# Kernel tuning notes

Hardware: AMD Instinct MI355X
Metric: run time of the kernel (lower is better)

The kernel has to match this reference:

```python
import jax, jax.numpy as jnp
import numpy as np

EMBED_DIM = 1024
NUM_HEADS = 16
HEAD_DIM = EMBED_DIM // NUM_HEADS
LAMBDA_ENTANGLE = 0.35


def setup_inputs() -> dict:
    key = jax.random.key(0)
    ks = jax.random.split(key, 10)
    B, S, D = 2, 2048, EMBED_DIM
    init = 1.0 / np.sqrt(D)  # mimic nn.Linear uniform init scale
    x = jax.random.normal(ks[0], (B, S, D), dtype=jnp.float32)
    Wq = jax.random.uniform(ks[1], (D, D), jnp.float32, -init, init)
    bq = jax.random.uniform(ks[2], (D,), jnp.float32, -init, init)
    Wk = jax.random.uniform(ks[3], (D, D), jnp.float32, -init, init)
    bk = jax.random.uniform(ks[4], (D,), jnp.float32, -init, init)
    Wv = jax.random.uniform(ks[5], (D, D), jnp.float32, -init, init)
    bv = jax.random.uniform(ks[6], (D,), jnp.float32, -init, init)
    Wo = jax.random.uniform(ks[7], (D, D), jnp.float32, -init, init)
    bo = jax.random.uniform(ks[8], (D,), jnp.float32, -init, init)
    J_attn = jax.random.normal(ks[9], (NUM_HEADS, HEAD_DIM, HEAD_DIM), dtype=jnp.float32) * 0.02
    lambda_attn = jnp.asarray(LAMBDA_ENTANGLE, dtype=jnp.float32)
    return {"x": x, "Wq": Wq, "bq": bq, "Wk": Wk, "bk": bk, "Wv": Wv, "bv": bv,
            "Wo": Wo, "bo": bo, "J_attn": J_attn, "lambda_attn": lambda_attn}


def reference(x, Wq, bq, Wk, bk, Wv, bv, Wo, bo, J_attn, lambda_attn):
    B, S, D = x.shape
    H, Hd = NUM_HEADS, HEAD_DIM
    scale = jnp.sqrt(jnp.asarray(Hd, dtype=x.dtype))

    def heads(W, b):
        # (B,S,D) @ (D,D) + b -> (B,H,S,Hd)
        y = jnp.einsum('bsd,ed->bse', x, W) + b
        return y.reshape(B, S, H, Hd).transpose(0, 2, 1, 3)

    Q = heads(Wq, bq)
    K = heads(Wk, bk)
    V = heads(Wv, bv)

    scores = jnp.einsum('bhid,bhjd->bhij', Q, K) / scale
    # bilinear entanglement correction: tanh(Q) J tanh(K)^T
    QJ = jnp.einsum('bhid,hde->bhie', jnp.tanh(Q), J_attn)  # (B,H,S,Hd)
    delta = jnp.einsum('bhie,bhje->bhij', QJ, jnp.tanh(K))
    scores = scores + lambda_attn * delta

    causal = jnp.triu(jnp.ones((S, S), dtype=bool), k=1)
    scores = jnp.where(causal, -jnp.inf, scores)

    probs = jax.nn.softmax(scores, axis=-1)
    out = jnp.einsum('bhij,bhjd->bhid', probs, V)  # (B,H,S,Hd)
    out = out.transpose(0, 2, 1, 3).reshape(B, S, D)
    return jnp.einsum('bsd,ed->bse', out, Wo) + bo
```

## Files before the change

### kernel.cpp

```cpp
#include <hip/hip_runtime.h>
#include <hip/hip_bf16.h>

typedef unsigned short u16;
typedef __bf16 bf16x8 __attribute__((ext_vector_type(8)));
typedef float f32x4 __attribute__((ext_vector_type(4)));
typedef unsigned short u16x4 __attribute__((ext_vector_type(4)));

#define MFMA16(a, b, c) __builtin_amdgcn_mfma_f32_16x16x32_bf16(a, b, c, 0, 0, 0)

#define EMB 1024
#define SEQ 2048
#define NH 16
#define HD 64
#define LOG2E 1.4426950408889634f

#define GLOAD_LDS16(g, l) __builtin_amdgcn_global_load_lds( \
    (const __attribute__((address_space(1))) unsigned int*)(g), \
    (__attribute__((address_space(3))) unsigned int*)(l), 16, 0, 0)

__device__ __forceinline__ float b2f(u16 u) {
    union { unsigned int i; float f; } v; v.i = ((unsigned int)u) << 16; return v.f;
}
__device__ __forceinline__ u16 f2b(float f) {
    __hip_bfloat16 h = __float2bfloat16(f);
    return *reinterpret_cast<u16*>(&h);
}
__device__ __forceinline__ u16x4 pack4(float a, float b, float c, float d) {
    union { __hip_bfloat162 h2[2]; u16x4 u; } r;
    r.h2[0] = __float22bfloat162_rn(float2{a, b});
    r.h2[1] = __float22bfloat162_rn(float2{c, d});
    return r.u;
}
__device__ __forceinline__ bf16x8 ldfrag(const u16* p) {
    return *reinterpret_cast<const bf16x8*>(p);
}
__device__ __forceinline__ bf16x8 cvt8(const float* p) {
    const float4 a = *reinterpret_cast<const float4*>(p);
    const float4 b = *reinterpret_cast<const float4*>(p + 4);
    union { u16x4 q[2]; bf16x8 v; } r;
    r.q[0] = pack4(a.x, a.y, a.z, a.w);
    r.q[1] = pack4(b.x, b.y, b.z, b.w);
    return r.v;
}
__device__ __forceinline__ float fast_tanh(float x) {
    float t = __builtin_amdgcn_exp2f(x * (2.0f * LOG2E));
    return 1.0f - 2.0f * __builtin_amdgcn_rcpf(t + 1.0f);
}

__global__ __launch_bounds__(256) void cvt_all(
        const float* __restrict__ x,  const float* __restrict__ Wq,
        const float* __restrict__ Wk, const float* __restrict__ Wv,
        const float* __restrict__ Wo, const float* __restrict__ J,
        u16* __restrict__ dst)
{
    size_t i = ((size_t)blockIdx.x * 256 + threadIdx.x) * 8;
    const float* src; size_t off; u16* d;
    if (i < 4194304) { src = x; off = i; d = dst + i; }
    else if (i < 8388608) {
        size_t j = i - 4194304; int w = (int)(j >> 20); off = j & 1048575;
        src = (w == 0) ? Wq : (w == 1) ? Wk : (w == 2) ? Wv : Wo;
        d = dst + i;
    } else {
        off = i - 8388608; src = J; d = dst + 29360128 + off;
    }
    *(bf16x8*)d = cvt8(src + off);
}

template<int MI>
__global__ __launch_bounds__(256, 4) void gemm_epi(
        const u16* __restrict__ A,
        const u16* __restrict__ W0, const float* __restrict__ B0,
        const u16* __restrict__ W1, const float* __restrict__ B1,
        const u16* __restrict__ W2, const float* __restrict__ B2,
        const float* __restrict__ lam, const u16* __restrict__ Jb,
        u16* __restrict__ Qa, u16* __restrict__ Ka, u16* __restrict__ Vt,
        float* __restrict__ out, int modeBase)
{
    const int mode = modeBase + blockIdx.z;
    const u16* W; const float* bias;
    if (blockIdx.z == 0)      { W = W0; bias = B0; }
    else if (blockIdx.z == 1) { W = W1; bias = B1; }
    else                      { W = W2; bias = B2; }

    __shared__ __attribute__((aligned(16))) u16 sA[MI * 32 * 64];
    __shared__ __attribute__((aligned(16))) u16 sB[128 * 64];

    const int t = threadIdx.x;
    const int w = t >> 6, L = t & 63;
    const int wm = w >> 1, wn = w & 1;
    const int lr = L & 15, lq = L >> 4;
    const int wbase = t & 192;
    const int m0 = blockIdx.y * (MI * 32), n0 = blockIdx.x * 128;

    f32x4 acc[MI][4];
#pragma unroll
    for (int i = 0; i < MI; i++)
#pragma unroll
        for (int j = 0; j < 4; j++) { f32x4 z = {0.f, 0.f, 0.f, 0.f}; acc[i][j] = z; }

    for (int k0 = 0; k0 < EMB; k0 += 64) {
        __syncthreads();
#pragma unroll
        for (int q = 0; q < MI; q++) {
            int c = q * 256 + t;
            int row = c >> 3, cc = c & 7;
            int col8 = cc ^ (row & 7);
            GLOAD_LDS16(&A[(size_t)(m0 + row) * EMB + k0 + col8 * 8],
                        &sA[(q * 256 + wbase) * 8]);
        }
#pragma unroll
        for (int q = 0; q < 4; q++) {
            int c = q * 256 + t;
            int row = c >> 3, cc = c & 7;
            int col8 = cc ^ (row & 7);
            GLOAD_LDS16(&W[(size_t)(n0 + row) * EMB + k0 + col8 * 8],
                        &sB[(q * 256 + wbase) * 8]);
        }
        __syncthreads();
#pragma unroll
        for (int s = 0; s < 2; s++) {
            bf16x8 af[MI], bfr[4];
#pragma unroll
            for (int mi = 0; mi < MI; mi++) {
                int row = wm * (MI * 16) + mi * 16 + lr;
                af[mi] = ldfrag(&sA[(row * 8 + ((s * 4 + lq) ^ (row & 7))) * 8]);
            }
#pragma unroll
            for (int ni = 0; ni < 4; ni++) {
                int row = wn * 64 + ni * 16 + lr;
                bfr[ni] = ldfrag(&sB[(row * 8 + ((s * 4 + lq) ^ (row & 7))) * 8]);
            }
#pragma unroll
            for (int mi = 0; mi < MI; mi++)
#pragma unroll
                for (int ni = 0; ni < 4; ni++)
                    acc[mi][ni] = MFMA16(bfr[ni], af[mi], acc[mi][ni]);
        }
    }

    if (mode == 1) __syncthreads();
    u16* sU = (w < 2) ? &sA[(size_t)w * 4096] : &sB[(size_t)(w - 2) * 4096];

    const float lamf = lam[0];
    const float qsc = 0.125f * LOG2E, lsc = lamf * LOG2E;
#pragma unroll
    for (int mi = 0; mi < MI; mi++)
#pragma unroll
        for (int ni = 0; ni < 4; ni++) {
            const int sg = m0 + wm * (MI * 16) + mi * 16 + lr;
            const int ng = n0 + wn * 64 + ni * 16 + lq * 4;
            const float4 bv4 = *(const float4*)&bias[ng];
            const float v0 = acc[mi][ni][0] + bv4.x;
            const float v1 = acc[mi][ni][1] + bv4.y;
            const float v2 = acc[mi][ni][2] + bv4.z;
            const float v3 = acc[mi][ni][3] + bv4.w;
            if (mode == 3) {
                float4 o = {v0, v1, v2, v3};
                *(float4*)&out[(size_t)sg * EMB + ng] = o;
            } else {
                const int b = sg >> 11, s0 = sg & 2047;
                const int h = ng >> 6, d0 = ng & 63;
                if (mode == 0) {
                    size_t i128 = ((size_t)(b * NH + h) * SEQ + s0) * 128 + d0;
                    *(u16x4*)&Qa[i128] = pack4(v0 * qsc, v1 * qsc, v2 * qsc, v3 * qsc);
                    *(u16x4*)&Qa[i128 + 64] =
                        pack4(lsc * fast_tanh(v0), lsc * fast_tanh(v1),
                              lsc * fast_tanh(v2), lsc * fast_tanh(v3));
                } else if (mode == 1) {
                    *(u16x4*)&Ka[((size_t)(b * NH + h) * SEQ + s0) * 128 + d0] =
                        pack4(v0, v1, v2, v3);
                    const int sl = mi * 16 + lr;
                    const int chunk = (d0 >> 3) ^ (sl & 7);
                    *(u16x4*)&sU[sl * 64 + chunk * 8 + (d0 & 7)] =
                        pack4(fast_tanh(v0), fast_tanh(v1),
                              fast_tanh(v2), fast_tanh(v3));
                } else {
#pragma unroll
                    for (int r = 0; r < 4; r++) {
                        float vr = (r == 0) ? v0 : (r == 1) ? v1 : (r == 2) ? v2 : v3;
                        Vt[((size_t)(b * NH + h) * HD + d0 + r) * SEQ + s0] = f2b(vr);
                    }
                }
            }
        }

    if (mode == 1) {
        const int hn = (n0 >> 6) + wn;
        const u16* Jh = Jb + (size_t)hn * 4096;
        bf16x8 jf[4][2];
#pragma unroll
        for (int nt = 0; nt < 4; nt++)
#pragma unroll
            for (int s2 = 0; s2 < 2; s2++)
                jf[nt][s2] = ldfrag(&Jh[(nt * 16 + lr) * 64 + s2 * 32 + lq * 8]);
#pragma unroll
        for (int rt2 = 0; rt2 < 4; rt2++) {
            int r64 = rt2 * 16 + lr;
            bf16x8 a0 = ldfrag(&sU[r64 * 64 + ((0 + lq) ^ (r64 & 7)) * 8]);
            bf16x8 a1 = ldfrag(&sU[r64 * 64 + ((4 + lq) ^ (r64 & 7)) * 8]);
            const int grow = m0 + wm * 64 + rt2 * 16 + lr;
            const int bb = grow >> 11, ss = grow & 2047;
            const size_t kbase = ((size_t)(bb * NH + hn) * SEQ + ss) * 128 + 64;
#pragma unroll
            for (int nt = 0; nt < 4; nt++) {
                f32x4 acc2 = {0.f, 0.f, 0.f, 0.f};
                acc2 = MFMA16(jf[nt][0], a0, acc2);
                acc2 = MFMA16(jf[nt][1], a1, acc2);
                *(u16x4*)&Ka[kbase + nt * 16 + lq * 4] =
                    pack4(acc2[0], acc2[1], acc2[2], acc2[3]);
            }
        }
    }
}

__global__ __launch_bounds__(512) void flash(
        const u16* __restrict__ Qa, const u16* __restrict__ Ka,
        const u16* __restrict__ Vt, u16* __restrict__ attn)
{
    __shared__ __attribute__((aligned(16))) u16 sK[2][128 * 128];
    __shared__ __attribute__((aligned(16))) u16 sVt[2][64 * 128];
    __shared__ __attribute__((aligned(16))) u16 sP[128 * 136];
    __shared__ float sLs[2][4][64][2];

    const int t = threadIdx.x, w = t >> 6, L = t & 63, lr = L & 15, lq = L >> 4;
    const int wq = w & 3, wk = w >> 2;
    const int bh = blockIdx.x & 31, p = blockIdx.x >> 5;
    const int i_l = wq * 16 + lr;
    const u16* Kbase = Ka + (size_t)bh * SEQ * 128;
    const u16* Vbase = Vt + (size_t)bh * HD * SEQ;
    const int b = bh >> 4, h = bh & 15;
    float* sOt = reinterpret_cast<float*>(sK);

    const u16* kq[4];
#pragma unroll
    for (int q = 0; q < 4; q++) {
        int c = q * 512 + t;
        int row = c >> 4, cc = c & 15;
        kq[q] = Kbase + (size_t)row * 128 + (cc ^ (row & 15)) * 8;
    }
    const u16* vq[2];
#pragma unroll
    for (int q = 0; q < 2; q++) {
        int c = q * 512 + t;
        int d = c >> 4, cc = c & 15;
        vq[q] = Vbase + (size_t)d * SEQ + (cc ^ (d & 7)) * 8;
    }

#pragma unroll 1
    for (int seg = 0; seg < 2; seg++) {
        const int qt = seg ? 15 - p : p;
        const int qm = qt * 128;

        bf16x8 qf[2][4];
#pragma unroll
        for (int g = 0; g < 2; g++) {
            const u16* qrow = Qa + ((size_t)bh * SEQ + qm + g * 64 + i_l) * 128;
#pragma unroll
            for (int s = 0; s < 4; s++) qf[g][s] = ldfrag(qrow + s * 32 + lq * 8);
        }

        f32x4 Ot[2][4];
#pragma unroll
        for (int g = 0; g < 2; g++)
#pragma unroll
            for (int i = 0; i < 4; i++) { f32x4 z = {0.f, 0.f, 0.f, 0.f}; Ot[g][i] = z; }
        float lsum[2] = {0.f, 0.f};

        {
            int4 a0 = *(const int4*)kq[0];
            int4 a1 = *(const int4*)kq[1];
            int4 a2 = *(const int4*)kq[2];
            int4 a3 = *(const int4*)kq[3];
            int4 b0 = *(const int4*)vq[0];
            int4 b1 = *(const int4*)vq[1];
            *(int4*)&sK[0][(size_t)(0 * 512 + t) * 8] = a0;
            *(int4*)&sK[0][(size_t)(1 * 512 + t) * 8] = a1;
            *(int4*)&sK[0][(size_t)(2 * 512 + t) * 8] = a2;
            *(int4*)&sK[0][(size_t)(3 * 512 + t) * 8] = a3;
            *(int4*)&sVt[0][(size_t)(0 * 512 + t) * 8] = b0;
            *(int4*)&sVt[0][(size_t)(1 * 512 + t) * 8] = b1;
        }
        __syncthreads();

        int cur = 0;
        for (int kt = 0; kt <= qt; kt++) {
            const bool pf = kt < qt;
            int4 rk0, rk1, rk2, rk3, rv0, rv1;
            if (pf) {
                const int kn = (kt + 1) * 128;
                rk0 = *(const int4*)(kq[0] + (size_t)kn * 128);
                rk1 = *(const int4*)(kq[1] + (size_t)kn * 128);
                rk2 = *(const int4*)(kq[2] + (size_t)kn * 128);
                rk3 = *(const int4*)(kq[3] + (size_t)kn * 128);
                rv0 = *(const int4*)(vq[0] + kn);
                rv1 = *(const int4*)(vq[1] + kn);
            }
            const u16* sKc = sK[cur];
            const u16* sVc = sVt[cur];

            f32x4 sc[2][4];
#pragma unroll
            for (int g = 0; g < 2; g++)
#pragma unroll
                for (int m = 0; m < 4; m++) { f32x4 z = {0.f,0.f,0.f,0.f}; sc[g][m] = z; }
            __builtin_amdgcn_s_setprio(1);
#pragma unroll
            for (int mt2 = 0; mt2 < 4; mt2++) {
                int j = wk * 64 + mt2 * 16 + lr;
#pragma unroll
                for (int s = 0; s < 4; s++) {
                    bf16x8 kf = ldfrag(&sKc[(j * 16 + ((s * 4 + lq) ^ (j & 15))) * 8]);
                    sc[0][mt2] = MFMA16(kf, qf[0][s], sc[0][mt2]);
                    sc[1][mt2] = MFMA16(kf, qf[1][s], sc[1][mt2]);
                }
            }
            __builtin_amdgcn_s_setprio(0);
            if (kt == qt) {
#pragma unroll
                for (int mt2 = 0; mt2 < 4; mt2++)
#pragma unroll
                    for (int r = 0; r < 4; r++) {
                        int jj = wk * 64 + mt2 * 16 + lq * 4 + r;
                        if (jj > i_l)      sc[0][mt2][r] = -INFINITY;
                        if (jj > 64 + i_l) sc[1][mt2][r] = -INFINITY;
                    }
            }
#pragma unroll
            for (int g = 0; g < 2; g++) {
#pragma unroll
                for (int mt2 = 0; mt2 < 4; mt2++) {
                    float e0 = __builtin_amdgcn_exp2f(sc[g][mt2][0]);
                    float e1 = __builtin_amdgcn_exp2f(sc[g][mt2][1]);
                    float e2 = __builtin_amdgcn_exp2f(sc[g][mt2][2]);
                    float e3 = __builtin_amdgcn_exp2f(sc[g][mt2][3]);
                    lsum[g] += (e0 + e1) + (e2 + e3);
                    *(u16x4*)&sP[(g * 64 + i_l) * 136 + wk * 64 + mt2 * 16 + lq * 4] =
                        pack4(e0, e1, e2, e3);
                }
            }
            __builtin_amdgcn_s_setprio(1);
#pragma unroll
            for (int s2l = 0; s2l < 2; s2l++) {
                bf16x8 pf0 = ldfrag(&sP[(i_l) * 136 + wk * 64 + s2l * 32 + lq * 8]);
                bf16x8 pf1 = ldfrag(&sP[(64 + i_l) * 136 + wk * 64 + s2l * 32 + lq * 8]);
#pragma unroll
                for (int mt = 0; mt < 4; mt++) {
                    int d = mt * 16 + lr;
                    bf16x8 vf = ldfrag(
                        &sVc[(d * 16 + ((wk * 8 + s2l * 4 + lq) ^ (d & 7))) * 8]);
                    Ot[0][mt] = MFMA16(vf, pf0, Ot[0][mt]);
                    Ot[1][mt] = MFMA16(vf, pf1, Ot[1][mt]);
                }
            }
            __builtin_amdgcn_s_setprio(0);
            if (pf) {
                *(int4*)&sK[cur ^ 1][(size_t)(0 * 512 + t) * 8] = rk0;
                *(int4*)&sK[cur ^ 1][(size_t)(1 * 512 + t) * 8] = rk1;
                *(int4*)&sK[cur ^ 1][(size_t)(2 * 512 + t) * 8] = rk2;
                *(int4*)&sK[cur ^ 1][(size_t)(3 * 512 + t) * 8] = rk3;
                *(int4*)&sVt[cur ^ 1][(size_t)(0 * 512 + t) * 8] = rv0;
                *(int4*)&sVt[cur ^ 1][(size_t)(1 * 512 + t) * 8] = rv1;
            }
            __syncthreads();
            cur ^= 1;
        }

#pragma unroll
        for (int g = 0; g < 2; g++) {
            lsum[g] += __shfl_xor(lsum[g], 16);
            lsum[g] += __shfl_xor(lsum[g], 32);
            sLs[wk][wq][L][g] = lsum[g];
        }
        if (wk == 1) {
            float* dst = &sOt[wq * 64 + L];
#pragma unroll
            for (int g = 0; g < 2; g++)
#pragma unroll
                for (int mt = 0; mt < 4; mt++)
#pragma unroll
                    for (int r = 0; r < 4; r++)
                        dst[256 * (g * 16 + mt * 4 + r)] = Ot[g][mt][r];
        }
        __syncthreads();
        if (wk == 0) {
            const float* src = &sOt[wq * 64 + L];
#pragma unroll
            for (int g = 0; g < 2; g++) {
                float ls = lsum[g] + sLs[1][wq][L][g];
                const float r0 = __builtin_amdgcn_rcpf(ls);
                const float inv = r0 * (2.0f - ls * r0);
                const size_t base =
                    ((size_t)(b * SEQ + qm + g * 64 + i_l)) * EMB + h * HD;
#pragma unroll
                for (int mt = 0; mt < 4; mt++)
                    *(u16x4*)&attn[base + mt * 16 + lq * 4] = pack4(
                        (Ot[g][mt][0] + src[256 * (g * 16 + mt * 4 + 0)]) * inv,
                        (Ot[g][mt][1] + src[256 * (g * 16 + mt * 4 + 1)]) * inv,
                        (Ot[g][mt][2] + src[256 * (g * 16 + mt * 4 + 2)]) * inv,
                        (Ot[g][mt][3] + src[256 * (g * 16 + mt * 4 + 3)]) * inv);
            }
        }
        __syncthreads();
    }
}

extern "C" void kernel_launch(void* const* d_in, const int* in_sizes, int n_in,
                              void* d_out, int out_size, void* d_ws, size_t ws_size,
                              hipStream_t stream)
{
    const float* x   = (const float*)d_in[0];
    const float* Wq  = (const float*)d_in[1];
    const float* bq  = (const float*)d_in[2];
    const float* Wk  = (const float*)d_in[3];
    const float* bk  = (const float*)d_in[4];
    const float* Wv  = (const float*)d_in[5];
    const float* bv  = (const float*)d_in[6];
    const float* Wo  = (const float*)d_in[7];
    const float* bo  = (const float*)d_in[8];
    const float* J   = (const float*)d_in[9];
    const float* lam = (const float*)d_in[10];

    u16* ws  = (u16*)d_ws;
    u16* xb  = ws;
    u16* Wqb = xb  + (size_t)4096 * 1024;
    u16* Wkb = Wqb + (size_t)1024 * 1024;
    u16* Wvb = Wkb + (size_t)1024 * 1024;
    u16* Wob = Wvb + (size_t)1024 * 1024;
    u16* Qa  = Wob + (size_t)1024 * 1024;
    u16* Ka  = Qa  + (size_t)32 * 2048 * 128;
    u16* Vt  = Ka  + (size_t)32 * 2048 * 128;
    u16* Jb  = Vt  + (size_t)32 * 64 * 2048;
    u16* attn = xb;
    float* dout = (float*)d_out;

    dim3 blk(256);
    cvt_all<<<dim3(4128), blk, 0, stream>>>(x, Wq, Wk, Wv, Wo, J, ws);
    gemm_epi<4><<<dim3(8, 32, 3), blk, 0, stream>>>(
        xb, Wqb, bq, Wkb, bk, Wvb, bv, lam, Jb, Qa, Ka, Vt, dout, 0);
    flash<<<dim3(256), dim3(512), 0, stream>>>(Qa, Ka, Vt, attn);
    gemm_epi<2><<<dim3(8, 64, 1), blk, 0, stream>>>(
        attn, Wob, bo, Wob, bo, Wob, bo, lam, Jb, Qa, Ka, Vt, dout, 3);
}
```

Before: 184.7 us.

## Double-buffer GEMM tiles via register staging to overlap loads with MFMA

After: 287.0 us. +55.4%, slower.

```diff
diff --git a/kernel.cpp b/kernel.cpp
--- a/kernel.cpp
+++ b/kernel.cpp
@@ -13,10 +13,6 @@
 #define NH 16
 #define HD 64
 #define LOG2E 1.4426950408889634f
-
-#define GLOAD_LDS16(g, l) __builtin_amdgcn_global_load_lds( \
-    (const __attribute__((address_space(1))) unsigned int*)(g), \
-    (__attribute__((address_space(3))) unsigned int*)(l), 16, 0, 0)
 
 __device__ __forceinline__ float b2f(u16 u) {
     union { unsigned int i; float f; } v; v.i = ((unsigned int)u) << 16; return v.f;
@@ -67,7 +63,7 @@
 }
 
 template<int MI>
-__global__ __launch_bounds__(256, 4) void gemm_epi(
+__global__ __launch_bounds__(256, (MI == 4 ? 2 : 3)) void gemm_epi(
         const u16* __restrict__ A,
         const u16* __restrict__ W0, const float* __restrict__ B0,
         const u16* __restrict__ W1, const float* __restrict__ B1,
@@ -82,53 +78,73 @@
     else if (blockIdx.z == 1) { W = W1; bias = B1; }
     else                      { W = W2; bias = B2; }
 
-    __shared__ __attribute__((aligned(16))) u16 sA[MI * 32 * 64];
-    __shared__ __attribute__((aligned(16))) u16 sB[128 * 64];
+    __shared__ __attribute__((aligned(16))) u16 sA[2][MI * 32 * 64];
+    __shared__ __attribute__((aligned(16))) u16 sB[2][128 * 64];
 
     const int t = threadIdx.x;
     const int w = t >> 6, L = t & 63;
     const int wm = w >> 1, wn = w & 1;
     const int lr = L & 15, lq = L >> 4;
-    const int wbase = t & 192;
     const int m0 = blockIdx.y * (MI * 32), n0 = blockIdx.x * 128;
 
+    const u16* aptr[MI];
+#pragma unroll
+    for (int q = 0; q < MI; q++) {
+        int c = q * 256 + t;
+        int row = c >> 3, col8 = (c & 7) ^ (row & 7);
+        aptr[q] = &A[(size_t)(m0 + row) * EMB + col8 * 8];
+    }
+    const u16* bptr[4];
+#pragma unroll
+    for (int q = 0; q < 4; q++) {
+        int c = q * 256 + t;
+        int row = c >> 3, col8 = (c & 7) ^ (row & 7);
+        bptr[q] = &W[(size_t)(n0 + row) * EMB + col8 * 8];
+    }
+
     f32x4 acc[MI][4];
 #pragma unroll
     for (int i = 0; i < MI; i++)
 #pragma unroll
         for (int j = 0; j < 4; j++) { f32x4 z = {0.f, 0.f, 0.f, 0.f}; acc[i][j] = z; }
 
+    {
+        int4 ra[MI], rb[4];
+#pragma unroll
+        for (int q = 0; q < MI; q++) ra[q] = *(const int4*)aptr[q];
+#pragma unroll
+        for (int q = 0; q < 4; q++)  rb[q] = *(const int4*)bptr[q];
+#pragma unroll
+        for (int q = 0; q < MI; q++) *(int4*)&sA[0][(size_t)(q * 256 + t) * 8] = ra[q];
+#pragma unroll
+        for (int q = 0; q < 4; q++)  *(int4*)&sB[0][(size_t)(q * 256 + t) * 8] = rb[q];
+    }
+    __syncthreads();
+
+    int cur = 0;
     for (int k0 = 0; k0 < EMB; k0 += 64) {
-        __syncthreads();
-#pragma unroll
-        for (int q = 0; q < MI; q++) {
-            int c = q * 256 + t;
-            int row = c >> 3, cc = c & 7;
-            int col8 = cc ^ (row & 7);
-            GLOAD_LDS16(&A[(size_t)(m0 + row) * EMB + k0 + col8 * 8],
-                        &sA[(q * 256 + wbase) * 8]);
-        }
-#pragma unroll
-        for (int q = 0; q < 4; q++) {
-            int c = q * 256 + t;
-            int row = c >> 3, cc = c & 7;
-            int col8 = cc ^ (row & 7);
-            GLOAD_LDS16(&W[(size_t)(n0 + row) * EMB + k0 + col8 * 8],
-                        &sB[(q * 256 + wbase) * 8]);
-        }
-        __syncthreads();
+        const bool pf = (k0 + 64) < EMB;
+        int4 ra[MI], rb[4];
+        if (pf) {
+#pragma unroll
+            for (int q = 0; q < MI; q++) ra[q] = *(const int4*)(aptr[q] + k0 + 64);
+#pragma unroll
+            for (int q = 0; q < 4; q++)  rb[q] = *(const int4*)(bptr[q] + k0 + 64);
+        }
+        const u16* sAc = sA[cur];
+        const u16* sBc = sB[cur];
 #pragma unroll
         for (int s = 0; s < 2; s++) {
             bf16x8 af[MI], bfr[4];
 #pragma unroll
             for (int mi = 0; mi < MI; mi++) {
                 int row = wm * (MI * 16) + mi * 16 + lr;
-                af[mi] = ldfrag(&sA[(row * 8 + ((s * 4 + lq) ^ (row & 7))) * 8]);
+                af[mi] = ldfrag(&sAc[(row * 8 + ((s * 4 + lq) ^ (row & 7))) * 8]);
             }
 #pragma unroll
             for (int ni = 0; ni < 4; ni++) {
                 int row = wn * 64 + ni * 16 + lr;
-                bfr[ni] = ldfrag(&sB[(row * 8 + ((s * 4 + lq) ^ (row & 7))) * 8]);
+                bfr[ni] = ldfrag(&sBc[(row * 8 + ((s * 4 + lq) ^ (row & 7))) * 8]);
             }
 #pragma unroll
             for (int mi = 0; mi < MI; mi++)
@@ -136,10 +152,19 @@
                 for (int ni = 0; ni < 4; ni++)
                     acc[mi][ni] = MFMA16(bfr[ni], af[mi], acc[mi][ni]);
         }
-    }
-
-    if (mode == 1) __syncthreads();
-    u16* sU = (w < 2) ? &sA[(size_t)w * 4096] : &sB[(size_t)(w - 2) * 4096];
+        if (pf) {
+#pragma unroll
+            for (int q = 0; q < MI; q++)
+                *(int4*)&sA[cur ^ 1][(size_t)(q * 256 + t) * 8] = ra[q];
+#pragma unroll
+            for (int q = 0; q < 4; q++)
+                *(int4*)&sB[cur ^ 1][(size_t)(q * 256 + t) * 8] = rb[q];
+        }
+        __syncthreads();
+        cur ^= 1;
+    }
+
+    u16* sU = (w < 2) ? &sA[0][(size_t)w * 4096] : &sB[0][(size_t)(w - 2) * 4096];
 
     const float lamf = lam[0];
     const float qsc = 0.125f * LOG2E, lsc = lamf * LOG2E;
@@ -185,6 +210,7 @@
         }
 
     if (mode == 1) {
+        __syncthreads();
         const int hn = (n0 >> 6) + wn;
         const u16* Jh = Jb + (size_t)hn * 4096;
         bf16x8 jf[4][2];
```

## Fuse Q/K/V projections into one kernel sharing the A tile with double-buffered LDS

Applied to the files above, without the earlier changes.

Result: slower. 221.4 us (+19.9%).

```diff
diff --git a/kernel.cpp b/kernel.cpp
--- a/kernel.cpp
+++ b/kernel.cpp
@@ -66,107 +66,131 @@
     *(bf16x8*)d = cvt8(src + off);
 }
 
-template<int MI>
-__global__ __launch_bounds__(256, 4) void gemm_epi(
+__global__ __launch_bounds__(512) void qkv_fused(
         const u16* __restrict__ A,
         const u16* __restrict__ W0, const float* __restrict__ B0,
         const u16* __restrict__ W1, const float* __restrict__ B1,
         const u16* __restrict__ W2, const float* __restrict__ B2,
         const float* __restrict__ lam, const u16* __restrict__ Jb,
-        u16* __restrict__ Qa, u16* __restrict__ Ka, u16* __restrict__ Vt,
-        float* __restrict__ out, int modeBase)
+        u16* __restrict__ Qa, u16* __restrict__ Ka, u16* __restrict__ Vt)
 {
-    const int mode = modeBase + blockIdx.z;
-    const u16* W; const float* bias;
-    if (blockIdx.z == 0)      { W = W0; bias = B0; }
-    else if (blockIdx.z == 1) { W = W1; bias = B1; }
-    else                      { W = W2; bias = B2; }
-
-    __shared__ __attribute__((aligned(16))) u16 sA[MI * 32 * 64];
-    __shared__ __attribute__((aligned(16))) u16 sB[128 * 64];
+    __shared__ __attribute__((aligned(16))) u16 sS[2][4][128 * 64];
 
     const int t = threadIdx.x;
     const int w = t >> 6, L = t & 63;
     const int wm = w >> 1, wn = w & 1;
     const int lr = L & 15, lq = L >> 4;
-    const int wbase = t & 192;
-    const int m0 = blockIdx.y * (MI * 32), n0 = blockIdx.x * 128;
-
-    f32x4 acc[MI][4];
-#pragma unroll
-    for (int i = 0; i < MI; i++)
-#pragma unroll
-        for (int j = 0; j < 4; j++) { f32x4 z = {0.f, 0.f, 0.f, 0.f}; acc[i][j] = z; }
-
+    const int m0 = blockIdx.y * 128, n0 = blockIdx.x * 128;
+
+    const int c0r = t >> 3,  c0o = ((t & 7) ^ (c0r & 7)) * 8;
+    const int c1  = 512 + t;
+    const int c1r = c1 >> 3, c1o = ((c1 & 7) ^ (c1r & 7)) * 8;
+    const u16* s0p[4], * s1p[4];
+    s0p[0] = A  + (size_t)(m0 + c0r) * EMB + c0o;
+    s0p[1] = W0 + (size_t)(n0 + c0r) * EMB + c0o;
+    s0p[2] = W1 + (size_t)(n0 + c0r) * EMB + c0o;
+    s0p[3] = W2 + (size_t)(n0 + c0r) * EMB + c0o;
+    s1p[0] = A  + (size_t)(m0 + c1r) * EMB + c1o;
+    s1p[1] = W0 + (size_t)(n0 + c1r) * EMB + c1o;
+    s1p[2] = W1 + (size_t)(n0 + c1r) * EMB + c1o;
+    s1p[3] = W2 + (size_t)(n0 + c1r) * EMB + c1o;
+
+    f32x4 acc[3][2][4];
+#pragma unroll
+    for (int z = 0; z < 3; z++)
+#pragma unroll
+        for (int i = 0; i < 2; i++)
+#pragma unroll
+            for (int j = 0; j < 4; j++) { f32x4 zr = {0.f,0.f,0.f,0.f}; acc[z][i][j] = zr; }
+
+    {
+        int4 r0[4], r1[4];
+#pragma unroll
+        for (int mat = 0; mat < 4; mat++) { r0[mat] = *(const int4*)s0p[mat];
+                                            r1[mat] = *(const int4*)s1p[mat]; }
+#pragma unroll
+        for (int mat = 0; mat < 4; mat++) {
+            *(int4*)&sS[0][mat][(size_t)t * 8]  = r0[mat];
+            *(int4*)&sS[0][mat][(size_t)c1 * 8] = r1[mat];
+        }
+    }
+    __syncthreads();
+
+    int cur = 0;
     for (int k0 = 0; k0 < EMB; k0 += 64) {
+        const bool pf = (k0 + 64) < EMB;
+        int4 r0[4], r1[4];
+        if (pf) {
+#pragma unroll
+            for (int mat = 0; mat < 4; mat++) {
+                r0[mat] = *(const int4*)(s0p[mat] + k0 + 64);
+                r1[mat] = *(const int4*)(s1p[mat] + k0 + 64);
+            }
+        }
+        __builtin_amdgcn_s_setprio(1);
+#pragma unroll
+        for (int s = 0; s < 2; s++) {
+            bf16x8 af[2];
+#pragma unroll
+            for (int mi = 0; mi < 2; mi++) {
+                int row = wm * 32 + mi * 16 + lr;
+                af[mi] = ldfrag(&sS[cur][0][(row * 8 + ((s * 4 + lq) ^ (row & 7))) * 8]);
+            }
+#pragma unroll
+            for (int z = 0; z < 3; z++) {
+                bf16x8 bfr[4];
+#pragma unroll
+                for (int ni = 0; ni < 4; ni++) {
+                    int row = wn * 64 + ni * 16 + lr;
+                    bfr[ni] = ldfrag(
+                        &sS[cur][1 + z][(row * 8 + ((s * 4 + lq) ^ (row & 7))) * 8]);
+                }
+#pragma unroll
+                for (int mi = 0; mi < 2; mi++)
+#pragma unroll
+                    for (int ni = 0; ni < 4; ni++)
+                        acc[z][mi][ni] = MFMA16(bfr[ni], af[mi], acc[z][mi][ni]);
+            }
+        }
+        __builtin_amdgcn_s_setprio(0);
+        if (pf) {
+#pragma unroll
+            for (int mat = 0; mat < 4; mat++) {
+                *(int4*)&sS[cur ^ 1][mat][(size_t)t * 8]  = r0[mat];
+                *(int4*)&sS[cur ^ 1][mat][(size_t)c1 * 8] = r1[mat];
+            }
+        }
         __syncthreads();
-#pragma unroll
-        for (int q = 0; q < MI; q++) {
-            int c = q * 256 + t;
-            int row = c >> 3, cc = c & 7;
-            int col8 = cc ^ (row & 7);
-            GLOAD_LDS16(&A[(size_t)(m0 + row) * EMB + k0 + col8 * 8],
-                        &sA[(q * 256 + wbase) * 8]);
-        }
-#pragma unroll
-        for (int q = 0; q < 4; q++) {
-            int c = q * 256 + t;
-            int row = c >> 3, cc = c & 7;
-            int col8 = cc ^ (row & 7);
-            GLOAD_LDS16(&W[(size_t)(n0 + row) * EMB + k0 + col8 * 8],
-                        &sB[(q * 256 + wbase) * 8]);
-        }
-        __syncthreads();
-#pragma unroll
-        for (int s = 0; s < 2; s++) {
-            bf16x8 af[MI], bfr[4];
-#pragma unroll
-            for (int mi = 0; mi < MI; mi++) {
-                int row = wm * (MI * 16) + mi * 16 + lr;
-                af[mi] = ldfrag(&sA[(row * 8 + ((s * 4 + lq) ^ (row & 7))) * 8]);
-            }
-#pragma unroll
-            for (int ni = 0; ni < 4; ni++) {
-                int row = wn * 64 + ni * 16 + lr;
-                bfr[ni] = ldfrag(&sB[(row * 8 + ((s * 4 + lq) ^ (row & 7))) * 8]);
-            }
-#pragma unroll
-            for (int mi = 0; mi < MI; mi++)
-#pragma unroll
-                for (int ni = 0; ni < 4; ni++)
-                    acc[mi][ni] = MFMA16(bfr[ni], af[mi], acc[mi][ni]);
-        }
-    }
-
-    if (mode == 1) __syncthreads();
-    u16* sU = (w < 2) ? &sA[(size_t)w * 4096] : &sB[(size_t)(w - 2) * 4096];
+        cur ^= 1;
+    }
+
+    u16* sU = &sS[0][0][(size_t)w * 2048];
 
     const float lamf = lam[0];
     const float qsc = 0.125f * LOG2E, lsc = lamf * LOG2E;
-#pragma unroll
-    for (int mi = 0; mi < MI; mi++)
-#pragma unroll
-        for (int ni = 0; ni < 4; ni++) {
-            const int sg = m0 + wm * (MI * 16) + mi * 16 + lr;
-            const int ng = n0 + wn * 64 + ni * 16 + lq * 4;
-            const float4 bv4 = *(const float4*)&bias[ng];
-            const float v0 = acc[mi][ni][0] + bv4.x;
-            const float v1 = acc[mi][ni][1] + bv4.y;
-            const float v2 = acc[mi][ni][2] + bv4.z;
-            const float v3 = acc[mi][ni][3] + bv4.w;
-            if (mode == 3) {
-                float4 o = {v0, v1, v2, v3};
-                *(float4*)&out[(size_t)sg * EMB + ng] = o;
-            } else {
+    const float* biases[3] = {B0, B1, B2};
+#pragma unroll
+    for (int z = 0; z < 3; z++)
+#pragma unroll
+        for (int mi = 0; mi < 2; mi++)
+#pragma unroll
+            for (int ni = 0; ni < 4; ni++) {
+                const int sg = m0 + wm * 32 + mi * 16 + lr;
+                const int ng = n0 + wn * 64 + ni * 16 + lq * 4;
+                const float4 bv4 = *(const float4*)&biases[z][ng];
+                const float v0 = acc[z][mi][ni][0] + bv4.x;
+                const float v1 = acc[z][mi][ni][1] + bv4.y;
+                const float v2 = acc[z][mi][ni][2] + bv4.z;
+                const float v3 = acc[z][mi][ni][3] + bv4.w;
                 const int b = sg >> 11, s0 = sg & 2047;
                 const int h = ng >> 6, d0 = ng & 63;
-                if (mode == 0) {
+                if (z == 0) {
                     size_t i128 = ((size_t)(b * NH + h) * SEQ + s0) * 128 + d0;
                     *(u16x4*)&Qa[i128] = pack4(v0 * qsc, v1 * qsc, v2 * qsc, v3 * qsc);
                     *(u16x4*)&Qa[i128 + 64] =
                         pack4(lsc * fast_tanh(v0), lsc * fast_tanh(v1),
                               lsc * fast_tanh(v2), lsc * fast_tanh(v3));
-                } else if (mode == 1) {
+                } else if (z == 1) {
                     *(u16x4*)&Ka[((size_t)(b * NH + h) * SEQ + s0) * 128 + d0] =
                         pack4(v0, v1, v2, v3);
                     const int sl = mi * 16 + lr;
@@ -182,9 +206,8 @@
                     }
                 }
             }
-        }
-
-    if (mode == 1) {
+
+    {
         const int hn = (n0 >> 6) + wn;
         const u16* Jh = Jb + (size_t)hn * 4096;
         bf16x8 jf[4][2];
@@ -194,11 +217,11 @@
             for (int s2 = 0; s2 < 2; s2++)
                 jf[nt][s2] = ldfrag(&Jh[(nt * 16 + lr) * 64 + s2 * 32 + lq * 8]);
 #pragma unroll
-        for (int rt2 = 0; rt2 < 4; rt2++) {
-            int r64 = rt2 * 16 + lr;
-            bf16x8 a0 = ldfrag(&sU[r64 * 64 + ((0 + lq) ^ (r64 & 7)) * 8]);
-            bf16x8 a1 = ldfrag(&sU[r64 * 64 + ((4 + lq) ^ (r64 & 7)) * 8]);
-            const int grow = m0 + wm * 64 + rt2 * 16 + lr;
+        for (int rt2 = 0; rt2 < 2; rt2++) {
+            const int r32 = rt2 * 16 + lr;
+            bf16x8 a0 = ldfrag(&sU[r32 * 64 + ((0 + lq) ^ (r32 & 7)) * 8]);
+            bf16x8 a1 = ldfrag(&sU[r32 * 64 + ((4 + lq) ^ (r32 & 7)) * 8]);
+            const int grow = m0 + wm * 32 + rt2 * 16 + lr;
             const int bb = grow >> 11, ss = grow & 2047;
             const size_t kbase = ((size_t)(bb * NH + hn) * SEQ + ss) * 128 + 64;
 #pragma unroll
@@ -211,6 +234,83 @@
             }
         }
     }
+}
+
+template<int MI>
+__global__ __launch_bounds__(256, 4) void gemm_epi(
+        const u16* __restrict__ A,
+        const u16* __restrict__ W0, const float* __restrict__ B0,
+        float* __restrict__ out)
+{
+    const u16* W = W0; const float* bias = B0;
+
+    __shared__ __attribute__((aligned(16))) u16 sA[MI * 32 * 64];
+    __shared__ __attribute__((aligned(16))) u16 sB[128 * 64];
+
+    const int t = threadIdx.x;
+    const int w = t >> 6, L = t & 63;
+    const int wm = w >> 1, wn = w & 1;
+    const int lr = L & 15, lq = L >> 4;
+    const int wbase = t & 192;
+    const int m0 = blockIdx.y * (MI * 32), n0 = blockIdx.x * 128;
+
+    f32x4 acc[MI][4];
+#pragma unroll
+    for (int i = 0; i < MI; i++)
+#pragma unroll
+        for (int j = 0; j < 4; j++) { f32x4 z = {0.f, 0.f, 0.f, 0.f}; acc[i][j] = z; }
+
+    for (int k0 = 0; k0 < EMB; k0 += 64) {
+        __syncthreads();
+#pragma unroll
+        for (int q = 0; q < MI; q++) {
+            int c = q * 256 + t;
+            int row = c >> 3, cc = c & 7;
+            int col8 = cc ^ (row & 7);
+            GLOAD_LDS16(&A[(size_t)(m0 + row) * EMB + k0 + col8 * 8],
+                        &sA[(q * 256 + wbase) * 8]);
+        }
+#pragma unroll
+        for (int q = 0; q < 4; q++) {
+            int c = q * 256 + t;
+            int row = c >> 3, cc = c & 7;
+            int col8 = cc ^ (row & 7);
+            GLOAD_LDS16(&W[(size_t)(n0 + row) * EMB + k0 + col8 * 8],
+                        &sB[(q * 256 + wbase) * 8]);
+        }
+        __syncthreads();
+#pragma unroll
+        for (int s = 0; s < 2; s++) {
+            bf16x8 af[MI], bfr[4];
+#pragma unroll
+            for (int mi = 0; mi < MI; mi++) {
+                int row = wm * (MI * 16) + mi * 16 + lr;
+                af[mi] = ldfrag(&sA[(row * 8 + ((s * 4 + lq) ^ (row & 7))) * 8]);
+            }
+#pragma unroll
+            for (int ni = 0; ni < 4; ni++) {
+                int row = wn * 64 + ni * 16 + lr;
+                bfr[ni] = ldfrag(&sB[(row * 8 + ((s * 4 + lq) ^ (row & 7))) * 8]);
+            }
+#pragma unroll
+            for (int mi = 0; mi < MI; mi++)
+#pragma unroll
+                for (int ni = 0; ni < 4; ni++)
+                    acc[mi][ni] = MFMA16(bfr[ni], af[mi], acc[mi][ni]);
+        }
+    }
+
+#pragma unroll
+    for (int mi = 0; mi < MI; mi++)
+#pragma unroll
+        for (int ni = 0; ni < 4; ni++) {
+            const int sg = m0 + wm * (MI * 16) + mi * 16 + lr;
+            const int ng = n0 + wn * 64 + ni * 16 + lq * 4;
+            const float4 bv4 = *(const float4*)&bias[ng];
+            float4 o = {acc[mi][ni][0] + bv4.x, acc[mi][ni][1] + bv4.y,
+                        acc[mi][ni][2] + bv4.z, acc[mi][ni][3] + bv4.w};
+            *(float4*)&out[(size_t)sg * EMB + ng] = o;
+        }
 }
 
 __global__ __launch_bounds__(512) void flash(
@@ -435,9 +535,8 @@
 
     dim3 blk(256);
     cvt_all<<<dim3(4128), blk, 0, stream>>>(x, Wq, Wk, Wv, Wo, J, ws);
-    gemm_epi<4><<<dim3(8, 32, 3), blk, 0, stream>>>(
-        xb, Wqb, bq, Wkb, bk, Wvb, bv, lam, Jb, Qa, Ka, Vt, dout, 0);
+    qkv_fused<<<dim3(8, 32), dim3(512), 0, stream>>>(
+        xb, Wqb, bq, Wkb, bk, Wvb, bv, lam, Jb, Qa, Ka, Vt);
     flash<<<dim3(256), dim3(512), 0, stream>>>(Qa, Ka, Vt, attn);
-    gemm_epi<2><<<dim3(8, 64, 1), blk, 0, stream>>>(
-        attn, Wob, bo, Wob, bo, Wob, bo, lam, Jb, Qa, Ka, Vt, dout, 3);
-}
+    gemm_epi<2><<<dim3(8, 64), blk, 0, stream>>>(attn, Wob, bo, dout);
+}
```
